# Kernel optimization log

Measured on AMD Instinct MI355X. Metric: run time of the kernel, lower is better.

Reference implementation:

```python
import jax, jax.numpy as jnp
import numpy as np

DIM = 2048
H = 16
DK = 128
DV = 128
KCONV = 4
EPS = 1e-6
B = 2
S = 2048
KD = H * DK  # 2048
VD = H * DV  # 2048


def setup_inputs() -> dict:
    key = jax.random.key(0)
    ks = jax.random.split(key, 16)
    sc = 0.02
    inp = {
        "x": jax.random.normal(ks[0], (B, S, DIM), dtype=jnp.float32),
        "Wq": jax.random.normal(ks[1], (KD, DIM), dtype=jnp.float32) * sc,
        "Wk": jax.random.normal(ks[2], (KD, DIM), dtype=jnp.float32) * sc,
        "Wv": jax.random.normal(ks[3], (VD, DIM), dtype=jnp.float32) * sc,
        "Wa": jax.random.normal(ks[4], (H, DIM), dtype=jnp.float32) * sc,
        "Wb": jax.random.normal(ks[5], (H, DIM), dtype=jnp.float32) * sc,
        "Wg": jax.random.normal(ks[6], (VD, DIM), dtype=jnp.float32) * sc,
        "Wo": jax.random.normal(ks[7], (DIM, VD), dtype=jnp.float32) * sc,
        "cw_q": jax.random.normal(ks[8], (KD, KCONV), dtype=jnp.float32) * 0.3,
        "cb_q": jnp.zeros((KD,), dtype=jnp.float32),
        "cw_k": jax.random.normal(ks[9], (KD, KCONV), dtype=jnp.float32) * 0.3,
        "cb_k": jnp.zeros((KD,), dtype=jnp.float32),
        "cw_v": jax.random.normal(ks[10], (VD, KCONV), dtype=jnp.float32) * 0.3,
        "cb_v": jnp.zeros((VD,), dtype=jnp.float32),
        "A_log": jnp.zeros((H,), dtype=jnp.float32),
        "dt_bias": jnp.zeros((H,), dtype=jnp.float32),
        "norm_w": jnp.ones((VD,), dtype=jnp.float32),
    }
    return inp


def _causal_conv(x, w, b):
    # x: [B, S, C]; w: [C, K]; b: [C]. Depthwise causal conv (zero init state) + SiLU.
    Bb, Ss, C = x.shape
    xp = jnp.pad(x, ((0, 0), (KCONV - 1, 0), (0, 0)))
    out = b
    for j in range(KCONV):
        out = out + xp[:, j:j + Ss, :] * w[:, j]
    return jax.nn.silu(out)


def _l2norm(x):
    n = jnp.sqrt(jnp.sum(x * x, axis=-1, keepdims=True))
    return x / jnp.maximum(n, 1e-12)


def _forward(x, Wq, Wk, Wv, Wa, Wb, Wg, Wo, cw_q, cb_q, cw_k, cb_k, cw_v, cb_v,
             A_log, dt_bias, norm_w):
    Bb, Ss, _ = x.shape
    q = _causal_conv(x @ Wq.T, cw_q, cb_q)  # [B,S,KD]
    k = _causal_conv(x @ Wk.T, cw_k, cb_k)
    v = _causal_conv(x @ Wv.T, cw_v, cb_v)

    a = x @ Wa.T  # [B,S,H]
    b = x @ Wb.T
    g = jnp.exp(-jnp.exp(A_log)[None, None, :] * jax.nn.softplus(a + dt_bias[None, None, :]))
    beta = jax.nn.sigmoid(b)

    q = _l2norm(q.reshape(Bb, Ss, H, DK))
    k = _l2norm(k.reshape(Bb, Ss, H, DK))
    v = v.reshape(Bb, Ss, H, DV)

    S0 = jnp.zeros((Bb, H, DK, DV), dtype=x.dtype)

    def step(Sstate, inputs):
        q_t, k_t, v_t, g_t, beta_t = inputs  # [B,H,DK],[B,H,DK],[B,H,DV],[B,H],[B,H]
        retrieved = jnp.einsum('bhkv,bhk->bhv', Sstate, k_t)
        error = v_t - g_t[..., None] * retrieved
        update = k_t[..., :, None] * (beta_t[..., None] * error)[..., None, :]
        Snew = g_t[..., None, None] * Sstate + update
        o_t = jnp.einsum('bhkv,bhk->bhv', Snew, q_t)
        return Snew, o_t

    # scan over time: move time axis to front
    xs = (q.transpose(1, 0, 2, 3), k.transpose(1, 0, 2, 3), v.transpose(1, 0, 2, 3),
          g.transpose(1, 0, 2), beta.transpose(1, 0, 2))
    _, o = jax.lax.scan(step, S0, xs)  # o: [S,B,H,DV]
    o = o.transpose(1, 0, 2, 3).reshape(Bb, Ss, VD)

    # RMSNorm
    o = o * jax.lax.rsqrt(jnp.mean(o * o, axis=-1, keepdims=True) + EPS) * norm_w
    o = o * jax.nn.silu(x @ Wg.T)
    return o @ Wo.T


def reference(x, Wq, Wk, Wv, Wa, Wb, Wg, Wo, cw_q, cb_q, cw_k, cb_k, cw_v, cb_v,
              A_log, dt_bias, norm_w):
    return _forward(x, Wq, Wk, Wv, Wa, Wb, Wg, Wo, cw_q, cb_q, cw_k, cb_k,
                    cw_v, cb_v, A_log, dt_bias, norm_w)
```

## Files before the change

kernel.cpp:

```cpp
#include <hip/hip_runtime.h>

#define S_LEN   2048
#define NH      16
#define DIM     2048
#define KD      2048
#define VD      2048
#define MB      1048576ull
#define CT      64
#define NC      32

typedef short  short8  __attribute__((ext_vector_type(8)));
typedef short  short4v __attribute__((ext_vector_type(4)));
typedef float  floatx4 __attribute__((ext_vector_type(4)));

#define MFMA(a, b, c) __builtin_amdgcn_mfma_f32_16x16x32_bf16((a), (b), (c), 0, 0, 0)

__device__ inline short f2bf(float x) {
    unsigned u = __float_as_uint(x);
    unsigned r = (u + 0x7fffu + ((u >> 16) & 1u)) >> 16;
    return (short)r;
}
__device__ inline float bf2f(short s) {
    return __uint_as_float(((unsigned)(unsigned short)s) << 16);
}
__device__ inline float silu_f(float x) { return x / (1.f + __expf(-x)); }

__device__ inline short8 neg8(short8 a) {
    unsigned* p = (unsigned*)&a;
    p[0] ^= 0x80008000u; p[1] ^= 0x80008000u;
    p[2] ^= 0x80008000u; p[3] ^= 0x80008000u;
    return a;
}

__device__ inline void load_lds16(const void* g, void* l) {
    __builtin_amdgcn_global_load_lds(
        (const __attribute__((address_space(1))) unsigned int*)g,
        (__attribute__((address_space(3))) unsigned int*)l, 16, 0, 0);
}

__device__ inline void store_c(float* C, size_t idx, float v) { C[idx] = v; }
__device__ inline void store_c(short* C, size_t idx, float v) { C[idx] = f2bf(v); }

__device__ __forceinline__ void lds_barrier() {
    asm volatile("s_waitcnt lgkmcnt(0)" ::: "memory");
    __builtin_amdgcn_s_barrier();
}

__device__ __forceinline__ void boundary_barrier() {
    asm volatile("s_waitcnt lgkmcnt(0)" ::: "memory");
    __builtin_amdgcn_s_barrier();
    asm volatile("" ::: "memory");
}

#define VM(n_) asm volatile("s_waitcnt vmcnt(" #n_ ")" ::: "memory");

__global__ __launch_bounds__(256) void cvt_all_kernel(
    const float* __restrict__ x,  const float* __restrict__ Wq,
    const float* __restrict__ Wk, const float* __restrict__ Wv,
    const float* __restrict__ Wg, const float* __restrict__ Wo,
    short* __restrict__ xb,  short* __restrict__ Wqb, short* __restrict__ Wkb,
    short* __restrict__ Wvb, short* __restrict__ Wgb, short* __restrict__ Wob) {
    const float* in; short* out; int n8;
    switch (blockIdx.y) {
        case 0:  in = x;  out = xb;  n8 = 1048576; break;
        case 1:  in = Wq; out = Wqb; n8 = 524288;  break;
        case 2:  in = Wk; out = Wkb; n8 = 524288;  break;
        case 3:  in = Wv; out = Wvb; n8 = 524288;  break;
        case 4:  in = Wg; out = Wgb; n8 = 524288;  break;
        default: in = Wo; out = Wob; n8 = 524288;  break;
    }
    int i = blockIdx.x * 256 + threadIdx.x;
    if (i >= n8) return;
    float4 a = ((const float4*)in)[2 * i];
    float4 b = ((const float4*)in)[2 * i + 1];
    short8 o;
    o[0] = f2bf(a.x); o[1] = f2bf(a.y); o[2] = f2bf(a.z); o[3] = f2bf(a.w);
    o[4] = f2bf(b.x); o[5] = f2bf(b.y); o[6] = f2bf(b.z); o[7] = f2bf(b.w);
    ((short8*)out)[i] = o;
}


#define STAGE8(s_, isB_)                                                     \
    {                                                                        \
        const char* gsrc = (isB_) ? (const char*)Bw : (const char*)A;        \
        int t0 = (isB_) ? n0 : m0;                                           \
        char* dbase = smem + ((s_) & 3) * 32768 + (isB_) * 16384;            \
        _Pragma("unroll")                                                    \
        for (int ld = 0; ld < 2; ++ld) {                                     \
            int ch = ld * 8 + wave;                                          \
            int Pl = (ch << 10) + (lane << 4);                               \
            int Q  = Pl ^ (((lane >> 3) & 3) << 4);                          \
            const char* src = gsrc + ((size_t)(t0 + (Q >> 6)) << 12)         \
                              + ((size_t)(s_) << 6) + (Q & 63);              \
            load_lds16(src, dbase + (ch << 10));                             \
        }                                                                    \
    }

#define RD_AF(dst_, s_, qm_)                                                 \
    {                                                                        \
        const char* sb_ = smem + ((s_) & 3) * 32768;                         \
        _Pragma("unroll")                                                    \
        for (int mf = 0; mf < 4; ++mf)                                       \
            dst_[mf] = *(const short8*)(sb_ +                                \
                ((rowA_base + (qm_) * 64 + mf * 16) << 6) + qsw);            \
    }

#define RD_BF(dst_, s_)                                                      \
    {                                                                        \
        const char* sb_ = smem + ((s_) & 3) * 32768 + 16384;                 \
        _Pragma("unroll")                                                    \
        for (int nf = 0; nf < 4; ++nf)                                       \
            dst_[nf] = *(const short8*)(sb_ +                                \
                ((rowB_base + nf * 16) << 6) + qsw);                         \
    }

#define MM(qm_, af_, bf_)                                                    \
    {                                                                        \
        __builtin_amdgcn_s_setprio(1);                                       \
        _Pragma("unroll")                                                    \
        for (int mf = 0; mf < 4; ++mf)                                       \
            _Pragma("unroll")                                                \
            for (int nf = 0; nf < 4; ++nf)                                   \
                acc[(qm_) * 4 + mf][nf] =                                    \
                    MFMA(af_[mf], bf_[nf], acc[(qm_) * 4 + mf][nf]);         \
        __builtin_amdgcn_s_setprio(0);                                       \
    }

template <typename OutT>
__device__ __forceinline__ void gemm8_tile(const short* __restrict__ A,
                                           const short* __restrict__ Bw,
                                           OutT* __restrict__ C, char* smem) {
    int x  = blockIdx.x;
    int xs = (x & 7) * 16 + (x >> 3);
    int m0 = (xs >> 3) * 256;
    int n0 = (xs & 7) * 256;
    int tid  = threadIdx.x;
    int wave = tid >> 6, lane = tid & 63;
    int l16  = lane & 15, quad = lane >> 4;
    int wm = wave >> 2, wn = wave & 3;
    int qsw = ((quad ^ ((l16 >> 1) & 3)) << 4);
    int rowA_base = wm * 128 + l16;
    int rowB_base = wn * 64 + l16;

    floatx4 acc[8][4];
#pragma unroll
    for (int i = 0; i < 8; ++i)
#pragma unroll
        for (int j = 0; j < 4; ++j) acc[i][j] = (floatx4){0.f, 0.f, 0.f, 0.f};
    short8 af0[4], af1[4], bfA[4], bfB[4];

    STAGE8(0, 0) STAGE8(0, 1)
    STAGE8(1, 0) STAGE8(1, 1)
    STAGE8(2, 0) STAGE8(2, 1)
    VM(8)
    boundary_barrier();
    RD_AF(af0, 0, 0) RD_BF(bfA, 0)

#pragma unroll 1
    for (int sp = 0; sp < 60; sp += 2) {
        STAGE8(sp + 3, 0)
        RD_AF(af1, sp, 1)
        MM(0, af0, bfA)
        STAGE8(sp + 3, 1)
        VM(8)
        boundary_barrier();
        RD_AF(af0, sp + 1, 0) RD_BF(bfB, sp + 1)
        MM(1, af1, bfA)
        STAGE8(sp + 4, 0)
        RD_AF(af1, sp + 1, 1)
        MM(0, af0, bfB)
        STAGE8(sp + 4, 1)
        VM(8)
        boundary_barrier();
        RD_AF(af0, sp + 2, 0) RD_BF(bfA, sp + 2)
        MM(1, af1, bfB)
    }

    STAGE8(63, 0)
    RD_AF(af1, 60, 1)
    MM(0, af0, bfA)
    STAGE8(63, 1)
    VM(8)
    boundary_barrier();
    RD_AF(af0, 61, 0) RD_BF(bfB, 61)
    MM(1, af1, bfA)
    RD_AF(af1, 61, 1)
    MM(0, af0, bfB)
    VM(4)
    boundary_barrier();
    RD_AF(af0, 62, 0) RD_BF(bfA, 62)
    MM(1, af1, bfB)
    RD_AF(af1, 62, 1)
    MM(0, af0, bfA)
    VM(0)
    boundary_barrier();
    RD_AF(af0, 63, 0) RD_BF(bfB, 63)
    MM(1, af1, bfA)
    RD_AF(af1, 63, 1)
    MM(0, af0, bfB)
    MM(1, af1, bfB)

#pragma unroll
    for (int i = 0; i < 8; ++i) {
        int row0 = m0 + wm * 128 + (i >> 2) * 64 + (i & 3) * 16 + quad * 4;
#pragma unroll
        for (int nf = 0; nf < 4; ++nf) {
            int col = n0 + wn * 64 + nf * 16 + l16;
#pragma unroll
            for (int r = 0; r < 4; ++r)
                store_c(C, (size_t)(row0 + r) * 2048 + col, acc[i][nf][r]);
        }
    }
}

__global__ __launch_bounds__(512, 2) void gemm8_qkvg(const short* __restrict__ A,
    const short* __restrict__ B0, const short* __restrict__ B1,
    const short* __restrict__ B2, const short* __restrict__ B3,
    short* __restrict__ C0, short* __restrict__ C1,
    short* __restrict__ C2, short* __restrict__ C3) {
    extern __shared__ char smem[];
    const short* Bw; short* C;
    switch (blockIdx.z) {
        case 0:  Bw = B0; C = C0; break;
        case 1:  Bw = B1; C = C1; break;
        case 2:  Bw = B2; C = C2; break;
        default: Bw = B3; C = C3; break;
    }
    gemm8_tile<short>(A, Bw, C, smem);
}

__global__ __launch_bounds__(512, 2) void gemm8_out(const short* __restrict__ A,
    const short* __restrict__ Bw, float* __restrict__ C) {
    extern __shared__ char smem[];
    gemm8_tile<float>(A, Bw, C, smem);
}

__global__ __launch_bounds__(256) void ab_kernel(const float* __restrict__ x,
    const float* __restrict__ Wa, const float* __restrict__ Wb,
    const float* __restrict__ Alog, const float* __restrict__ dtb,
    float* __restrict__ gdec, float* __restrict__ beta) {
    int t = threadIdx.x;
    int wave = t >> 6, lane = t & 63;
    int l16 = lane & 15, grp = lane >> 4;
    int m0 = (blockIdx.x * 4 + wave) * 2;
    const float4* x0 = (const float4*)(x + (size_t)m0 * DIM);
    const float4* x1 = (const float4*)(x + (size_t)(m0 + 1) * DIM);

#pragma unroll 1
    for (int p = 0; p < 8; ++p) {
        int c = p * 4 + grp;
        const float4* wr = (const float4*)((c < 16) ? (Wa + (size_t)c * DIM)
                                                    : (Wb + (size_t)(c - 16) * DIM));
        float s0 = 0.f, s1 = 0.f;
#pragma unroll 8
        for (int j = 0; j < 32; ++j) {
            float4 wv = wr[j * 16 + l16];
            float4 a0 = x0[j * 16 + l16];
            float4 a1 = x1[j * 16 + l16];
            s0 += a0.x * wv.x + a0.y * wv.y + a0.z * wv.z + a0.w * wv.w;
            s1 += a1.x * wv.x + a1.y * wv.y + a1.z * wv.z + a1.w * wv.w;
        }
#pragma unroll
        for (int off = 1; off < 16; off <<= 1) {
            s0 += __shfl_xor(s0, off);
            s1 += __shfl_xor(s1, off);
        }
        if (l16 < 2) {
            int m = m0 + l16;
            float sv = l16 ? s1 : s0;
            if (c < 16) {
                float sp = sv + dtb[c];
                float softp = (sp > 20.f) ? sp : log1pf(expf(sp));
                gdec[(size_t)m * NH + c] = expf(-expf(Alog[c]) * softp);
            } else {
                beta[(size_t)m * NH + (c - 16)] = 1.f / (1.f + expf(-sv));
            }
        }
    }
}

__global__ __launch_bounds__(256) void conv_kernel(
    const short* __restrict__ qr, const short* __restrict__ kr, const short* __restrict__ vr,
    const float* __restrict__ cwq, const float* __restrict__ cbq,
    const float* __restrict__ cwk, const float* __restrict__ cbk,
    const float* __restrict__ cwv, const float* __restrict__ cbv,
    short* __restrict__ qn, short* __restrict__ kn, short* __restrict__ vc) {
    int gw   = blockIdx.x * 4 + (threadIdx.x >> 6);
    int lane = threadIdx.x & 63;
    int h  = gw & (NH - 1);
    int m  = gw >> 4;
    int tt = m & (S_LEN - 1);
    int c  = h * 128 + lane * 2;
    size_t rowbase = (size_t)m * KD + c;

    float4 wq0 = ((const float4*)cwq)[c], wq1 = ((const float4*)cwq)[c + 1];
    float4 wk0 = ((const float4*)cwk)[c], wk1 = ((const float4*)cwk)[c + 1];
    float4 wv0 = ((const float4*)cwv)[c], wv1 = ((const float4*)cwv)[c + 1];
    float q0 = cbq[c], q1 = cbq[c + 1];
    float k0 = cbk[c], k1 = cbk[c + 1];
    float v0 = cbv[c], v1 = cbv[c + 1];
    const float* wq0a = (const float*)&wq0; const float* wq1a = (const float*)&wq1;
    const float* wk0a = (const float*)&wk0; const float* wk1a = (const float*)&wk1;
    const float* wv0a = (const float*)&wv0; const float* wv1a = (const float*)&wv1;
#pragma unroll
    for (int j = 0; j < 4; ++j) {
        int ts = tt - 3 + j;
        if (ts >= 0) {
            long long rb = (long long)rowbase + (long long)(j - 3) * KD;
            unsigned uq = *(const unsigned*)(qr + rb);
            unsigned uk = *(const unsigned*)(kr + rb);
            unsigned uv = *(const unsigned*)(vr + rb);
            q0 += bf2f((short)(uq & 0xffff)) * wq0a[j]; q1 += bf2f((short)(uq >> 16)) * wq1a[j];
            k0 += bf2f((short)(uk & 0xffff)) * wk0a[j]; k1 += bf2f((short)(uk >> 16)) * wk1a[j];
            v0 += bf2f((short)(uv & 0xffff)) * wv0a[j]; v1 += bf2f((short)(uv >> 16)) * wv1a[j];
        }
    }
    q0 = silu_f(q0); q1 = silu_f(q1);
    k0 = silu_f(k0); k1 = silu_f(k1);
    v0 = silu_f(v0); v1 = silu_f(v1);

    float sq = q0 * q0 + q1 * q1;
    float sk = k0 * k0 + k1 * k1;
#pragma unroll
    for (int off = 1; off < 64; off <<= 1) {
        sq += __shfl_xor(sq, off);
        sk += __shfl_xor(sk, off);
    }
    float iq = 1.f / fmaxf(sqrtf(sq), 1e-12f);
    float ik = 1.f / fmaxf(sqrtf(sk), 1e-12f);
    unsigned oq = (unsigned)(unsigned short)f2bf(q0 * iq) | ((unsigned)(unsigned short)f2bf(q1 * iq) << 16);
    unsigned ok = (unsigned)(unsigned short)f2bf(k0 * ik) | ((unsigned)(unsigned short)f2bf(k1 * ik) << 16);
    unsigned ov = (unsigned)(unsigned short)f2bf(v0)      | ((unsigned)(unsigned short)f2bf(v1)      << 16);
    *(unsigned*)(qn + rowbase) = oq;
    *(unsigned*)(kn + rowbase) = ok;
    *(unsigned*)(vc + rowbase) = ov;
}

__global__ __launch_bounds__(256) void solve_kernel(
    const short* __restrict__ kn, const short* __restrict__ vn,
    const float* __restrict__ gdec, const float* __restrict__ beta,
    short* __restrict__ UvT, short* __restrict__ Tk) {
    __shared__ short Pn[64][72];
    __shared__ short Pt[64][72];
    __shared__ short UT[128][72];
    __shared__ float Ls[64];
    __shared__ float Bs[64];

    int wg   = blockIdx.x;
    int half = wg & 1;
    int c    = (wg >> 1) & 31;
    int bh   = wg >> 6;
    int b = bh >> 4, h = bh & 15;
    int tid = threadIdx.x;
    int wave = tid >> 6, lane = tid & 63;
    int quad = lane >> 4, l16 = lane & 15;

    const short* Kb = kn + ((size_t)(b * S_LEN + c * CT)) * KD + h * 128;
    const short* Vb = vn + ((size_t)(b * S_LEN + c * CT)) * KD + h * 128;

    if (wave == 0) {
        float lg = __logf(gdec[((size_t)(b * S_LEN + c * CT) + lane) * NH + h]);
#pragma unroll
        for (int off = 1; off < 64; off <<= 1) {
            float y = __shfl_up(lg, off);
            if (lane >= off) lg += y;
        }
        Ls[lane] = lg;
        Bs[lane] = beta[((size_t)(b * S_LEN + c * CT) + lane) * NH + h];
    }
    __syncthreads();

    {
        floatx4 acc[4];
#pragma unroll
        for (int i = 0; i < 4; ++i) acc[i] = (floatx4){0.f, 0.f, 0.f, 0.f};
        for (int ks = 0; ks < 4; ++ks) {
            short8 af = *(const short8*)(Kb + (size_t)(wave * 16 + l16) * KD + ks * 32 + quad * 8);
#pragma unroll
            for (int it = 0; it < 4; ++it) {
                short8 bf = *(const short8*)(Kb + (size_t)(it * 16 + l16) * KD + ks * 32 + quad * 8);
                acc[it] = MFMA(af, bf, acc[it]);
            }
        }
#pragma unroll
        for (int it = 0; it < 4; ++it) {
            int icol = it * 16 + l16;
#pragma unroll
            for (int r = 0; r < 4; ++r) {
                int trow = wave * 16 + quad * 4 + r;
                float v = 0.f;
                if (icol < trow) v = -Bs[trow] * __expf(Ls[trow] - Ls[icol]) * acc[it][r];
                short bv = f2bf(v);
                Pn[trow][icol] = bv;
                Pt[icol][trow] = bv;
            }
        }
    }

    {
        const short* src = half ? Kb : Vb;
        int tr = tid >> 2, seg = (tid & 3) * 32;
        float s = Bs[tr] * (half ? __expf(Ls[tr]) : 1.f);
#pragma unroll
        for (int j = 0; j < 4; ++j) {
            short8 d = *(const short8*)(src + (size_t)tr * KD + seg + j * 8);
#pragma unroll
            for (int e = 0; e < 8; ++e)
                UT[seg + j * 8 + e][tr] = f2bf(bf2f(d[e]) * s);
        }
    }
    __syncthreads();

    for (int iter = 0; iter < 6; ++iter) {
        floatx4 acc[8];
#pragma unroll
        for (int nt = 0; nt < 8; ++nt) {
            short4v u4 = *(const short4v*)&UT[nt * 16 + l16][wave * 16 + quad * 4];
            floatx4 a;
#pragma unroll
            for (int e = 0; e < 4; ++e) a[e] = bf2f(u4[e]);
            acc[nt] = a;
        }
        for (int ks = 0; ks < 2; ++ks) {
            short8 af = *(const short8*)&Pn[wave * 16 + l16][ks * 32 + quad * 8];
#pragma unroll
            for (int nt = 0; nt < 8; ++nt) {
                short8 bf = *(const short8*)&UT[nt * 16 + l16][ks * 32 + quad * 8];
                acc[nt] = MFMA(af, bf, acc[nt]);
            }
        }
        __syncthreads();
        if (iter < 5) {
#pragma unroll
            for (int nt = 0; nt < 8; ++nt) {
                short4v w4;
#pragma unroll
                for (int e = 0; e < 4; ++e) w4[e] = f2bf(acc[nt][e]);
                *(short4v*)&UT[nt * 16 + l16][wave * 16 + quad * 4] = w4;
            }
            floatx4 pacc[4];
#pragma unroll
            for (int it = 0; it < 4; ++it) pacc[it] = (floatx4){0.f, 0.f, 0.f, 0.f};
            for (int ks = 0; ks < 2; ++ks) {
                short8 paf = *(const short8*)&Pn[wave * 16 + l16][ks * 32 + quad * 8];
#pragma unroll
                for (int it = 0; it < 4; ++it) {
                    short8 pbf = *(const short8*)&Pt[it * 16 + l16][ks * 32 + quad * 8];
                    pacc[it] = MFMA(paf, pbf, pacc[it]);
                }
            }
            __syncthreads();
#pragma unroll
            for (int it = 0; it < 4; ++it) {
                int icol = it * 16 + l16;
#pragma unroll
                for (int r = 0; r < 4; ++r) {
                    int trow = wave * 16 + quad * 4 + r;
                    short bv = f2bf(pacc[it][r]);
                    Pn[trow][icol] = bv;
                    Pt[icol][trow] = bv;
                }
            }
            __syncthreads();
        } else {
            size_t cb = (size_t)(bh * NC + c);
            if (half == 0) {
                int usw = (((wave * 2 + (quad >> 1)) ^ (l16 & 7)) << 3) + ((quad & 1) << 2);
#pragma unroll
                for (int nt = 0; nt < 8; ++nt) {
                    short4v w4;
#pragma unroll
                    for (int e = 0; e < 4; ++e) w4[e] = f2bf(acc[nt][e]);
                    *(short4v*)(UvT + (cb * 128 + nt * 16 + l16) * 64 + usw) = w4;
                }
            } else {
#pragma unroll
                for (int nt = 0; nt < 8; ++nt)
#pragma unroll
                    for (int r = 0; r < 4; ++r) {
                        int trow = wave * 16 + quad * 4 + r;
                        int colsw = (((nt * 2 + (l16 >> 3)) ^ (trow & 7)) << 3) + (l16 & 7);
                        Tk[(cb * 64 + trow) * 128 + colsw] = f2bf(acc[nt][r]);
                    }
            }
        }
    }
}

__global__ __launch_bounds__(256) void prepb_kernel(
    const short* __restrict__ qn, const short* __restrict__ kn,
    const float* __restrict__ gdec,
    short* __restrict__ Wb_, short* __restrict__ Qg,
    short* __restrict__ KtT, float* __restrict__ gam63) {
    __shared__ short KT[128][72];
    __shared__ float Ls[64];
    int wg = blockIdx.x;
    int c = wg & 31, bh = wg >> 5;
    int b = bh >> 4, h = bh & 15;
    int tid = threadIdx.x, wave = tid >> 6, lane = tid & 63;
    int quad = lane >> 4, l16 = lane & 15;
    const short* Qb = qn + ((size_t)(b * S_LEN + c * CT)) * KD + h * 128;
    const short* Kb = kn + ((size_t)(b * S_LEN + c * CT)) * KD + h * 128;

    if (wave == 0) {
        float lg = __logf(gdec[((size_t)(b * S_LEN + c * CT) + lane) * NH + h]);
#pragma unroll
        for (int off = 1; off < 64; off <<= 1) {
            float y = __shfl_up(lg, off);
            if (lane >= off) lg += y;
        }
        Ls[lane] = lg;
    }
    __syncthreads();
    size_t cb = (size_t)(bh * NC + c);
    if (tid == 0) gam63[cb] = __expf(Ls[63]);

    {
        floatx4 acc[4];
#pragma unroll
        for (int i = 0; i < 4; ++i) acc[i] = (floatx4){0.f, 0.f, 0.f, 0.f};
        for (int ks = 0; ks < 4; ++ks) {
            short8 af = *(const short8*)(Qb + (size_t)(wave * 16 + l16) * KD + ks * 32 + quad * 8);
#pragma unroll
            for (int it = 0; it < 4; ++it) {
                short8 bf = *(const short8*)(Kb + (size_t)(it * 16 + l16) * KD + ks * 32 + quad * 8);
                acc[it] = MFMA(af, bf, acc[it]);
            }
        }
#pragma unroll
        for (int it = 0; it < 4; ++it) {
            int icol = it * 16 + l16;
#pragma unroll
            for (int r = 0; r < 4; ++r) {
                int trow = wave * 16 + quad * 4 + r;
                float v = (icol <= trow) ? __expf(Ls[trow] - Ls[icol]) * acc[it][r] : 0.f;
                int colsw = (((it * 2 + (l16 >> 3)) ^ (trow & 7)) << 3) + (l16 & 7);
                Wb_[(cb * 64 + trow) * 64 + colsw] = f2bf(v);
            }
        }
    }

    {
        int tr = tid >> 2, seg = (tid & 3) * 32;
        float sq = __expf(Ls[tr]);
        float sk = __expf(Ls[63] - Ls[tr]);
#pragma unroll
        for (int j = 0; j < 4; ++j) {
            short8 dq = *(const short8*)(Qb + (size_t)tr * KD + seg + j * 8);
            short8 dk = *(const short8*)(Kb + (size_t)tr * KD + seg + j * 8);
            short8 oq;
#pragma unroll
            for (int e = 0; e < 8; ++e) {
                oq[e] = f2bf(bf2f(dq[e]) * sq);
                KT[seg + j * 8 + e][tr] = f2bf(bf2f(dk[e]) * sk);
            }
            int ch = (tid & 3) * 4 + j;
            *(short8*)(Qg + (cb * 64 + tr) * 128 + ((ch ^ (tr & 7)) << 3)) = oq;
        }
    }
    __syncthreads();
    {
        int dk = tid >> 1, seg = (tid & 1) * 32;
#pragma unroll
        for (int j = 0; j < 4; ++j) {
            short8 v = *(const short8*)&KT[dk][seg + j * 8];
            int ch = (tid & 1) * 4 + j;
            *(short8*)(KtT + (cb * 128 + dk) * 64 + ((ch ^ (dk & 7)) << 3)) = v;
        }
    }
}

__global__ __launch_bounds__(256, 1) void seq_kernel(
    const short* __restrict__ UvT, const short* __restrict__ Tk,
    const short* __restrict__ Wb_, const short* __restrict__ Qg,
    const short* __restrict__ KtT, const float* __restrict__ gam63,
    short* __restrict__ ob) {
    extern __shared__ char smem[];
    const int BUF = 65536;
    const int TKO = 0, QGO = 16384, KTO = 32768, UVO = 49152, WO = 57344;
    short (*ST)[136] = (short (*)[136])(smem + 131072);
    short (*UTs)[72] = (short (*)[72])(smem + 131072 + 17408);

    int wg = blockIdx.x;
    int vh = wg & 1, bh = wg >> 1;
    int b = bh >> 4, h = bh & 15;
    int tid = threadIdx.x, wave = tid >> 6, lane = tid & 63;
    int quad = lane >> 4, l16 = lane & 15;
    int swk = l16 & 7;

    for (int i = tid; i < 64 * 136; i += 256) ((short*)(smem + 131072))[i] = 0;
    floatx4 sacc[8];
#pragma unroll
    for (int i = 0; i < 8; ++i) sacc[i] = (floatx4){0.f, 0.f, 0.f, 0.f};

    size_t cb0 = (size_t)bh * NC;
    int row16 = wave * 16 + l16;
    int chq[4];
#pragma unroll
    for (int ks = 0; ks < 4; ++ks) chq[ks] = (((ks * 4 + quad) ^ swk) << 4);
    int uvoff = (((wave * 2 + (quad >> 1)) ^ swk) << 4) + ((quad & 1) << 3);

#define STAGE_CHUNK(bsel_, c_)                                                       \
    {                                                                                \
        char* dst = smem + (bsel_) * BUF;                                            \
        size_t cbs = cb0 + (c_);                                                     \
        const char* gt = (const char*)Tk  + cbs * 16384 + wave * 1024 + lane * 16;   \
        const char* gq = (const char*)Qg  + cbs * 16384 + wave * 1024 + lane * 16;   \
        const char* gk = (const char*)KtT + cbs * 16384 + wave * 1024 + lane * 16;   \
        const char* gu = (const char*)UvT + cbs * 16384 + (size_t)vh * 8192 + wave * 1024 + lane * 16; \
        const char* gw = (const char*)Wb_ + cbs * 8192  + wave * 1024 + lane * 16;   \
        _Pragma("unroll")                                                            \
        for (int it = 0; it < 4; ++it) {                                             \
            load_lds16(gt + it * 4096, dst + TKO + it * 4096 + wave * 1024);         \
            load_lds16(gq + it * 4096, dst + QGO + it * 4096 + wave * 1024);         \
            load_lds16(gk + it * 4096, dst + KTO + it * 4096 + wave * 1024);         \
        }                                                                            \
        _Pragma("unroll")                                                            \
        for (int it = 0; it < 2; ++it) {                                             \
            load_lds16(gu + it * 4096, dst + UVO + it * 4096 + wave * 1024);         \
            load_lds16(gw + it * 4096, dst + WO  + it * 4096 + wave * 1024);         \
        }                                                                            \
    }

    STAGE_CHUNK(0, 0)
    float gamA = gam63[cb0];
    __syncthreads();

#pragma unroll 1
    for (int c = 0; c < NC; ++c) {
        float gamN = 0.f;
        if (c + 1 < NC) {
            gamN = gam63[cb0 + c + 1];
            STAGE_CHUNK((c + 1) & 1, c + 1)
        }
        const char* bufc = smem + (c & 1) * BUF;

        floatx4 uacc[4], oacc[4];
#pragma unroll
        for (int vt = 0; vt < 4; ++vt) {
            short4v u4 = *(const short4v*)(bufc + UVO + (vt * 16 + l16) * 128 + uvoff);
            floatx4 a;
#pragma unroll
            for (int e = 0; e < 4; ++e) a[e] = bf2f(u4[e]);
            uacc[vt] = a;
            oacc[vt] = (floatx4){0.f, 0.f, 0.f, 0.f};
        }
#pragma unroll
        for (int ks = 0; ks < 4; ++ks) {
            short8 tkf = *(const short8*)(bufc + TKO + row16 * 256 + chq[ks]);
            short8 qgf = *(const short8*)(bufc + QGO + row16 * 256 + chq[ks]);
            short8 afT = neg8(tkf);
#pragma unroll
            for (int vt = 0; vt < 4; ++vt) {
                short8 bf = *(const short8*)&ST[vt * 16 + l16][ks * 32 + quad * 8];
                uacc[vt] = MFMA(afT, bf, uacc[vt]);
                oacc[vt] = MFMA(qgf, bf, oacc[vt]);
            }
        }
#pragma unroll
        for (int vt = 0; vt < 4; ++vt) {
            short4v w4;
#pragma unroll
            for (int e = 0; e < 4; ++e) w4[e] = f2bf(uacc[vt][e]);
            *(short4v*)&UTs[vt * 16 + l16][wave * 16 + quad * 4] = w4;
        }
        lds_barrier();
#pragma unroll
        for (int ks = 0; ks < 2; ++ks) {
            short8 wf = *(const short8*)(bufc + WO + row16 * 128 + chq[ks]);
#pragma unroll
            for (int vt = 0; vt < 4; ++vt) {
                short8 bf = *(const short8*)&UTs[vt * 16 + l16][ks * 32 + quad * 8];
                oacc[vt] = MFMA(wf, bf, oacc[vt]);
            }
        }
#pragma unroll
        for (int vt = 0; vt < 4; ++vt)
#pragma unroll
            for (int r = 0; r < 4; ++r) {
                int m = b * S_LEN + c * CT + wave * 16 + quad * 4 + r;
                ob[(size_t)m * VD + h * 128 + vh * 64 + vt * 16 + l16] = f2bf(oacc[vt][r]);
            }
#pragma unroll
        for (int dt = 0; dt < 8; ++dt)
#pragma unroll
            for (int e = 0; e < 4; ++e) sacc[dt][e] *= gamA;
#pragma unroll
        for (int ks = 0; ks < 2; ++ks) {
            short8 af = *(const short8*)&UTs[wave * 16 + l16][ks * 32 + quad * 8];
#pragma unroll
            for (int dt = 0; dt < 8; ++dt) {
                short8 ktf = *(const short8*)(bufc + KTO + (dt * 16 + l16) * 128 + chq[ks]);
                sacc[dt] = MFMA(af, ktf, sacc[dt]);
            }
        }
#pragma unroll
        for (int dt = 0; dt < 8; ++dt)
#pragma unroll
            for (int r = 0; r < 4; ++r)
                ST[wave * 16 + quad * 4 + r][dt * 16 + l16] = f2bf(sacc[dt][r]);

        if (c + 1 < NC) {
            asm volatile("s_waitcnt lgkmcnt(0)" ::: "memory");
            VM(16)
            __builtin_amdgcn_s_barrier();
        }
        gamA = gamN;
    }
#undef STAGE_CHUNK
}

__global__ __launch_bounds__(256) void rms_gate_kernel(
    const short* __restrict__ o, const short* __restrict__ graw,
    const float* __restrict__ nw, short* __restrict__ og) {
    __shared__ float red[4];
    int m = blockIdx.x, t = threadIdx.x;
    short8 a = ((const short8*)(o + (size_t)m * VD))[t];
    float av[8];
#pragma unroll
    for (int i = 0; i < 8; ++i) av[i] = bf2f(a[i]);
    float ss = 0.f;
#pragma unroll
    for (int i = 0; i < 8; ++i) ss += av[i] * av[i];
#pragma unroll
    for (int off = 1; off < 64; off <<= 1) ss += __shfl_xor(ss, off);
    if ((t & 63) == 0) red[t >> 6] = ss;
    __syncthreads();
    float tot = red[0] + red[1] + red[2] + red[3];
    float sc = rsqrtf(tot * (1.f / VD) + 1e-6f);
    short8 gv = ((const short8*)(graw + (size_t)m * VD))[t];
    float4 n0 = ((const float4*)nw)[2 * t];
    float4 n1 = ((const float4*)nw)[2 * t + 1];
    const float* na = (const float*)&n0;
    const float* nb = (const float*)&n1;
    short8 ov;
#pragma unroll
    for (int i = 0; i < 4; ++i) ov[i]     = f2bf(av[i]     * sc * na[i] * silu_f(bf2f(gv[i])));
#pragma unroll
    for (int i = 0; i < 4; ++i) ov[i + 4] = f2bf(av[i + 4] * sc * nb[i] * silu_f(bf2f(gv[i + 4])));
    ((short8*)(og + (size_t)m * VD))[t] = ov;
}

extern "C" void kernel_launch(void* const* d_in, const int* in_sizes, int n_in,
                              void* d_out, int out_size, void* d_ws, size_t ws_size,
                              hipStream_t stream) {
    const float* x    = (const float*)d_in[0];
    const float* Wq   = (const float*)d_in[1];
    const float* Wk   = (const float*)d_in[2];
    const float* Wv   = (const float*)d_in[3];
    const float* Wa   = (const float*)d_in[4];
    const float* Wb   = (const float*)d_in[5];
    const float* Wg   = (const float*)d_in[6];
    const float* Wo   = (const float*)d_in[7];
    const float* cwq  = (const float*)d_in[8];
    const float* cbq  = (const float*)d_in[9];
    const float* cwk  = (const float*)d_in[10];
    const float* cbk  = (const float*)d_in[11];
    const float* cwv  = (const float*)d_in[12];
    const float* cbv  = (const float*)d_in[13];
    const float* Alog = (const float*)d_in[14];
    const float* dtb  = (const float*)d_in[15];
    const float* nw   = (const float*)d_in[16];

    char* ws = (char*)d_ws;
    short* Wob = (short*)(ws);
    short* xb  = (short*)(ws + 8 * MB);
    short* Wqb = (short*)(ws + 24 * MB);
    short* Wkb = (short*)(ws + 32 * MB);
    short* Wvb = (short*)(ws + 40 * MB);
    short* Wgb = (short*)(ws + 48 * MB);
    short* qrb = (short*)(ws + 56 * MB);
    short* krb = (short*)(ws + 72 * MB);
    short* vrb = (short*)(ws + 88 * MB);
    short* grb = (short*)(ws + 104 * MB);
    short* qnb = (short*)(ws + 8 * MB);
    short* knb = (short*)(ws + 24 * MB);
    short* vnb = (short*)(ws + 40 * MB);
    float* gdec = (float*)(ws + 120 * MB);
    float* beta = (float*)(ws + 120 * MB + 262144);
    short* ob  = qrb;
    short* ogb = krb;
    short* UvT  = (short*)(ws + 121 * MB);
    short* Tkb  = (short*)(ws + 137 * MB);
    short* Wbuf = (short*)(ws + 153 * MB);
    short* Qgb  = (short*)(ws + 161 * MB);
    short* KtT  = (short*)(ws + 177 * MB);
    float* gm63 = (float*)(ws + 193 * MB);

    static bool attr_done = false;
    if (!attr_done) {
        hipFuncSetAttribute((const void*)gemm8_qkvg,
                            hipFuncAttributeMaxDynamicSharedMemorySize, 131072);
        hipFuncSetAttribute((const void*)gemm8_out,
                            hipFuncAttributeMaxDynamicSharedMemorySize, 131072);
        hipFuncSetAttribute((const void*)seq_kernel,
                            hipFuncAttributeMaxDynamicSharedMemorySize, 157696);
        attr_done = true;
    }

    cvt_all_kernel<<<dim3(4096, 6), 256, 0, stream>>>(x, Wq, Wk, Wv, Wg, Wo,
                                                      xb, Wqb, Wkb, Wvb, Wgb, Wob);

    ab_kernel<<<512, 256, 0, stream>>>(x, Wa, Wb, Alog, dtb, gdec, beta);

    gemm8_qkvg<<<dim3(128, 1, 4), 512, 131072, stream>>>(xb, Wqb, Wkb, Wvb, Wgb,
                                                         qrb, krb, vrb, grb);

    conv_kernel<<<16384, 256, 0, stream>>>(qrb, krb, vrb,
                                           cwq, cbq, cwk, cbk, cwv, cbv, qnb, knb, vnb);

    solve_kernel<<<2048, 256, 0, stream>>>(knb, vnb, gdec, beta, UvT, Tkb);
    prepb_kernel<<<1024, 256, 0, stream>>>(qnb, knb, gdec, Wbuf, Qgb, KtT, gm63);
    seq_kernel<<<64, 256, 157696, stream>>>(UvT, Tkb, Wbuf, Qgb, KtT, gm63, ob);

    rms_gate_kernel<<<4096, 256, 0, stream>>>(ob, grb, nw, ogb);

    gemm8_out<<<dim3(128, 1, 1), 512, 131072, stream>>>(ogb, Wob, (float*)d_out);
}
```

Measured before the change: 663.8 us.

## Use 128x256 tiles for output GEMM to double block count

Replaces the output projection GEMM, which used the shared 256x256-style tile path with 128 blocks, with a dedicated kernel using 128x256 tiles and 256 blocks, a 4-stage LDS pipeline, and a swizzled block order. On a GPU with 256 CUs, 128 blocks leave half the machine idle, so the aim is better occupancy for this 4096x2048x2048 GEMM. The cost is lower arithmetic intensity per tile, meaning more global and LDS traffic per FLOP.

```diff
diff --git a/kernel.cpp b/kernel.cpp
--- a/kernel.cpp
+++ b/kernel.cpp
@@ -229,10 +229,116 @@
     gemm8_tile<short>(A, Bw, C, smem);
 }
 
-__global__ __launch_bounds__(512, 2) void gemm8_out(const short* __restrict__ A,
+__global__ __launch_bounds__(512, 2) void gemm_out128(const short* __restrict__ A,
     const short* __restrict__ Bw, float* __restrict__ C) {
     extern __shared__ char smem[];
-    gemm8_tile<float>(A, Bw, C, smem);
+    int x   = blockIdx.x;
+    int swz = (x & 7) * 32 + (x >> 3);
+    int m0  = (swz >> 3) * 128;
+    int n0  = (swz & 7) * 256;
+    int tid = threadIdx.x;
+    int wave = tid >> 6, lane = tid & 63;
+    int l16 = lane & 15, quad = lane >> 4;
+    int wm = wave >> 2, wn = wave & 3;
+    int qsw = ((quad ^ ((l16 >> 1) & 3)) << 4);
+    int rowA = wm * 64 + l16;
+    int rowB = wn * 64 + l16;
+
+    floatx4 acc[4][4];
+#pragma unroll
+    for (int i = 0; i < 4; ++i)
+#pragma unroll
+        for (int j = 0; j < 4; ++j) acc[i][j] = (floatx4){0.f, 0.f, 0.f, 0.f};
+    short8 afA[4], bfA[4], afB[4], bfB[4];
+
+#define STG128(s_)                                                            \
+    {                                                                         \
+        char* dbase = smem + ((s_) & 3) * 24576;                              \
+        {                                                                     \
+            int D = (wave << 10) + (lane << 4);                               \
+            int Q = D ^ (((lane >> 3) & 3) << 4);                             \
+            const char* src = (const char*)A + ((size_t)(m0 + (Q >> 6)) << 12)\
+                              + ((size_t)(s_) << 6) + (Q & 63);               \
+            load_lds16(src, dbase + (wave << 10));                            \
+        }                                                                     \
+        _Pragma("unroll")                                                     \
+        for (int ld = 0; ld < 2; ++ld) {                                      \
+            int D = (ld << 13) + (wave << 10) + (lane << 4);                  \
+            int Q = D ^ (((lane >> 3) & 3) << 4);                             \
+            const char* src = (const char*)Bw + ((size_t)(n0 + (Q >> 6)) << 12)\
+                              + ((size_t)(s_) << 6) + (Q & 63);               \
+            load_lds16(src, dbase + 8192 + (ld << 13) + (wave << 10));        \
+        }                                                                     \
+    }
+
+#define RD128(af_, bf_, s_)                                                   \
+    {                                                                         \
+        const char* sb_ = smem + ((s_) & 3) * 24576;                          \
+        _Pragma("unroll")                                                     \
+        for (int f = 0; f < 4; ++f) {                                         \
+            af_[f] = *(const short8*)(sb_ + ((rowA + f * 16) << 6) + qsw);    \
+            bf_[f] = *(const short8*)(sb_ + 8192 + ((rowB + f * 16) << 6) + qsw); \
+        }                                                                     \
+    }
+
+#define MM128(af_, bf_)                                                       \
+    {                                                                         \
+        __builtin_amdgcn_s_setprio(1);                                        \
+        _Pragma("unroll")                                                     \
+        for (int i = 0; i < 4; ++i)                                           \
+            _Pragma("unroll")                                                 \
+            for (int j = 0; j < 4; ++j)                                       \
+                acc[i][j] = MFMA(af_[i], bf_[j], acc[i][j]);                  \
+        __builtin_amdgcn_s_setprio(0);                                        \
+    }
+
+    STG128(0) STG128(1) STG128(2)
+    VM(6)
+    boundary_barrier();
+    RD128(afA, bfA, 0)
+
+#pragma unroll 1
+    for (int s = 0; s < 60; s += 2) {
+        STG128(s + 3)
+        VM(6)
+        boundary_barrier();
+        RD128(afB, bfB, s + 1)
+        MM128(afA, bfA)
+        STG128(s + 4)
+        VM(6)
+        boundary_barrier();
+        RD128(afA, bfA, s + 2)
+        MM128(afB, bfB)
+    }
+    STG128(63)
+    VM(6)
+    boundary_barrier();
+    RD128(afB, bfB, 61)
+    MM128(afA, bfA)
+    VM(3)
+    boundary_barrier();
+    RD128(afA, bfA, 62)
+    MM128(afB, bfB)
+    VM(0)
+    boundary_barrier();
+    RD128(afB, bfB, 63)
+    MM128(afA, bfA)
+    MM128(afB, bfB)
+
+#pragma unroll
+    for (int i = 0; i < 4; ++i) {
+        int row0 = m0 + wm * 64 + i * 16 + quad * 4;
+#pragma unroll
+        for (int j = 0; j < 4; ++j) {
+            int col = n0 + wn * 64 + j * 16 + l16;
+#pragma unroll
+            for (int r = 0; r < 4; ++r)
+                C[(size_t)(row0 + r) * 2048 + col] = acc[i][j][r];
+        }
+    }
+#undef STG128
+#undef RD128
+#undef MM128
 }
 
 __global__ __launch_bounds__(256) void ab_kernel(const float* __restrict__ x,
@@ -791,8 +897,8 @@
     if (!attr_done) {
         hipFuncSetAttribute((const void*)gemm8_qkvg,
                             hipFuncAttributeMaxDynamicSharedMemorySize, 131072);
-        hipFuncSetAttribute((const void*)gemm8_out,
-                            hipFuncAttributeMaxDynamicSharedMemorySize, 131072);
+        hipFuncSetAttribute((const void*)gemm_out128,
+                            hipFuncAttributeMaxDynamicSharedMemorySize, 98304);
         hipFuncSetAttribute((const void*)seq_kernel,
                             hipFuncAttributeMaxDynamicSharedMemorySize, 157696);
         attr_done = true;
@@ -815,5 +921,5 @@
 
     rms_gate_kernel<<<4096, 256, 0, stream>>>(ob, grb, nw, ogb);
 
-    gemm8_out<<<dim3(128, 1, 1), 512, 131072, stream>>>(ogb, Wob, (float*)d_out);
-}
+    gemm_out128<<<256, 512, 98304, stream>>>(ogb, Wob, (float*)d_out);
+}
```

Result: faster. 632.9 us (-4.7%).
